# Performance work log

Measured on AMD Instinct MI355X. Metric: run time of the kernel, lower is better.

The kernel has to match this reference:

```python
import jax, jax.numpy as jnp
import numpy as np

N_NODES = 100000
N_EDGES = 1600000
DIM_IN, DIM_H, DIM_OUT = 64, 64, 16


def setup_inputs() -> dict:
    key = jax.random.key(0)
    ks = jax.random.split(key, 7)
    s = lambda d: 1.0 / np.sqrt(d)
    return {
        "x": jax.random.normal(ks[0], (N_NODES, DIM_IN), dtype=jnp.float32),
        "edge_index": jax.random.randint(ks[1], (2, N_EDGES), 0, N_NODES, dtype=jnp.int32),
        "W1l": jax.random.normal(ks[2], (DIM_IN, DIM_H), dtype=jnp.float32) * s(DIM_IN),
        "W1r": jax.random.normal(ks[3], (DIM_IN, DIM_H), dtype=jnp.float32) * s(DIM_IN),
        "b1": jnp.zeros((DIM_H,), dtype=jnp.float32),
        "W2l": jax.random.normal(ks[4], (DIM_H, DIM_OUT), dtype=jnp.float32) * s(DIM_H),
        "W2r": jax.random.normal(ks[5], (DIM_H, DIM_OUT), dtype=jnp.float32) * s(DIM_H),
        "b2": jnp.zeros((DIM_OUT,), dtype=jnp.float32),
    }


def _sage_conv(h, edge_index, Wl, Wr, b):
    # PyG SAGEConv (mean aggr): out = mean_{j in N(i)} h_j @ Wl + h_i @ Wr + b
    src, dst = edge_index[0], edge_index[1]
    n = h.shape[0]
    agg = jax.ops.segment_sum(h[src], dst, num_segments=n)          # [N, d]
    deg = jax.ops.segment_sum(jnp.ones_like(dst, dtype=h.dtype), dst, num_segments=n)
    mean = agg / jnp.maximum(deg, 1.0)[:, None]
    return mean @ Wl + h @ Wr + b


def reference(x, edge_index, W1l, W1r, b1, W2l, W2r, b2):
    h = jax.nn.relu(_sage_conv(x, edge_index, W1l, W1r, b1))
    # dropout(p=0.5) is identity in eval mode (training=False)
    h = _sage_conv(h, edge_index, W2l, W2r, b2)
    return jax.nn.log_softmax(h, axis=1)
```

## Files before the change

kernel.cpp:

```cpp
#include <hip/hip_runtime.h>
#include <cstdint>
#include <cstddef>


typedef float f32x4 __attribute__((ext_vector_type(4)));
typedef float f32x2 __attribute__((ext_vector_type(2)));
typedef short short8 __attribute__((ext_vector_type(8)));
typedef __bf16 bf16x8 __attribute__((ext_vector_type(8)));

#define BK 256
#define NBMAX 512
#define CAP 5120
#define TILE 8192

__device__ __forceinline__ unsigned f2bf(float f) {
    unsigned u = __float_as_uint(f);
    u += 0x7FFFu + ((u >> 16) & 1u);
    return u >> 16;
}

__device__ __forceinline__ f32x4 mfma16(short8 a, short8 b, f32x4 c) {
    return __builtin_amdgcn_mfma_f32_16x16x32_bf16(
        __builtin_bit_cast(bf16x8, a), __builtin_bit_cast(bf16x8, b), c, 0, 0, 0);
}

#define ACC2(r, alo, ahi)                     \
    alo += __uint_as_float((r) << 16);        \
    ahi += __uint_as_float(r);

#define ACCF8(w, i)                                                   \
    {                                                                 \
        f32x2 f0 = __builtin_amdgcn_cvt_pk_f32_fp8((w), false);       \
        f32x2 f1 = __builtin_amdgcn_cvt_pk_f32_fp8((w), true);        \
        acc[(i)] += f0.x; acc[(i) + 1] += f0.y;                       \
        acc[(i) + 2] += f1.x; acc[(i) + 3] += f1.y;                   \
    }

__global__ __launch_bounds__(512) void partprep_k(
    const int* __restrict__ ei, int* __restrict__ bcnt,
    unsigned* __restrict__ part, int E, int pblocks,
    const float* __restrict__ x, unsigned short* __restrict__ xb,
    unsigned char* __restrict__ xq, int n,
    const float* __restrict__ W1l, const float* __restrict__ W1r,
    const float* __restrict__ W2l, const float* __restrict__ W2r,
    unsigned short* __restrict__ bimg, int xblocks) {
    __shared__ int scn[NBMAX], sbase[NBMAX], lofs[NBMAX], cur[NBMAX];
    __shared__ unsigned stageW[TILE];
    __shared__ unsigned short stageB[TILE];
    int t = threadIdx.x;
    int bid = blockIdx.x;

    if (bid >= pblocks) {
        int cb = bid - pblocks;
        if (cb < xblocks) {
            int i = (cb * 512 + t) * 8;
            if (i >= n) return;
            const float4* xp = (const float4*)(x + i);
            float4 a = xp[0], b = xp[1];
            uint4 o;
            o.x = f2bf(a.x) | (f2bf(a.y) << 16);
            o.y = f2bf(a.z) | (f2bf(a.w) << 16);
            o.z = f2bf(b.x) | (f2bf(b.y) << 16);
            o.w = f2bf(b.z) | (f2bf(b.w) << 16);
            *(uint4*)(xb + i) = o;
            int w0 = __builtin_amdgcn_cvt_pk_fp8_f32(a.x, a.y, 0, false);
            w0 = __builtin_amdgcn_cvt_pk_fp8_f32(a.z, a.w, w0, true);
            int w1 = __builtin_amdgcn_cvt_pk_fp8_f32(b.x, b.y, 0, false);
            w1 = __builtin_amdgcn_cvt_pk_fp8_f32(b.z, b.w, w1, true);
            *(uint2*)(xq + i) = make_uint2((unsigned)w0, (unsigned)w1);
            return;
        }
        int e = (cb - xblocks) * 512 + t;
        if (e >= 20 * 64) return;
        int f = e >> 6, L = e & 63;
        int qd = L >> 4, m = L & 15;
        unsigned o[8];
        if (f < 16) {
            int kb = f >> 2, nb = f & 3;
            int n2 = nb * 16 + m;
#pragma unroll
            for (int j = 0; j < 8; ++j) {
                int k = kb * 32 + qd * 8 + j;
                float v = (k < 64) ? W1l[k * 64 + n2] : W1r[(k - 64) * 64 + n2];
                o[j] = f2bf(v);
            }
        } else {
            int g = f - 16;
            int kb = g >> 1, nb = g & 1;
#pragma unroll
            for (int j = 0; j < 8; ++j) {
                int k = kb * 32 + qd * 8 + j;
                float v = nb ? W2r[k * 16 + m] : W2l[k * 16 + m];
                o[j] = f2bf(v);
            }
        }
        uint4 pk;
        pk.x = o[0] | (o[1] << 16);
        pk.y = o[2] | (o[3] << 16);
        pk.z = o[4] | (o[5] << 16);
        pk.w = o[6] | (o[7] << 16);
        ((uint4*)bimg)[e] = pk;
        return;
    }

    int base = bid * TILE;
    cur[t] = 0;
    __syncthreads();
    int4 s4[4], d4[4];
#pragma unroll
    for (int i = 0; i < 4; ++i) {
        int e0 = base + (t + i * 512) * 4;
        if (e0 < E) {
            s4[i] = ((const int4*)ei)[e0 >> 2];
            d4[i] = ((const int4*)(ei + E))[e0 >> 2];
        } else {
            d4[i] = make_int4(-1, -1, -1, -1);
            s4[i] = make_int4(0, 0, 0, 0);
        }
    }
    int rk[16];
#pragma unroll
    for (int i = 0; i < 4; ++i) {
        int d[4] = {d4[i].x, d4[i].y, d4[i].z, d4[i].w};
#pragma unroll
        for (int u = 0; u < 4; ++u)
            rk[i * 4 + u] = (d[u] >= 0) ? atomicAdd(&cur[d[u] >> 8], 1) : 0;
    }
    __syncthreads();
    int own = cur[t];
    scn[t] = own;
    __syncthreads();
    for (int off = 1; off < NBMAX; off <<= 1) {
        int v = (t >= off) ? scn[t - off] : 0;
        __syncthreads();
        scn[t] += v;
        __syncthreads();
    }
    lofs[t] = scn[t] - own;
    if (own > 0) sbase[t] = atomicAdd(&bcnt[t], own);
    __syncthreads();
#pragma unroll
    for (int i = 0; i < 4; ++i) {
        int s[4] = {s4[i].x, s4[i].y, s4[i].z, s4[i].w};
        int d[4] = {d4[i].x, d4[i].y, d4[i].z, d4[i].w};
#pragma unroll
        for (int u = 0; u < 4; ++u) {
            if (d[u] < 0) continue;
            int b = d[u] >> 8;
            int pos = lofs[b] + rk[i * 4 + u];
            stageW[pos] = ((unsigned)(d[u] & (BK - 1)) << 17) | (unsigned)s[u];
            stageB[pos] = (unsigned short)b;
        }
    }
    __syncthreads();
    int tot = scn[NBMAX - 1];
    for (int q = t; q < tot; q += 512) {
        int b = stageB[q];
        part[b * CAP + sbase[b] + (q - lofs[b])] = stageW[q];
    }
}

__global__ __launch_bounds__(256) void csr_k(const unsigned* __restrict__ part,
                                             const int* __restrict__ bcnt,
                                             int* __restrict__ csr,
                                             int2* __restrict__ rowse, int N) {
    __shared__ int h[BK];
    __shared__ int s[BK];
    int b = blockIdx.x, t = threadIdx.x;
    int cnt = bcnt[b];
    int base = b * CAP;
    h[t] = 0;
    __syncthreads();
    for (int q = t; q < cnt; q += 256)
        atomicAdd(&h[(part[base + q] >> 17) & (BK - 1)], 1);
    __syncthreads();
    int own = h[t];
    s[t] = own;
    __syncthreads();
    for (int off = 1; off < BK; off <<= 1) {
        int v = (t >= off) ? s[t - off] : 0;
        __syncthreads();
        s[t] += v;
        __syncthreads();
    }
    int excl = s[t] - own;
    int node = b * BK + t;
    if (node < N) rowse[node] = make_int2(base + excl, base + excl + own);
    __syncthreads();
    h[t] = excl;
    __syncthreads();
    for (int q = t; q < cnt; q += 256) {
        unsigned w = part[base + q];
        int pos = atomicAdd(&h[(w >> 17) & (BK - 1)], 1);
        csr[base + pos] = (int)(w & 0x1FFFFu);
    }
}

__global__ __launch_bounds__(256, 6) void l1x(
    const unsigned short* __restrict__ xb, const unsigned char* __restrict__ xq,
    const int2* __restrict__ rowse, const int* __restrict__ csr,
    const unsigned short* __restrict__ bimg,
    const float* __restrict__ b1, const float* __restrict__ b2,
    unsigned short* __restrict__ p, float* __restrict__ q, int N) {
    __shared__ unsigned short mh[4][16][72];
    int t = threadIdx.x;
    int wave = t >> 6, lane = t & 63;
    int nodebase = blockIdx.x * 64 + wave * 16;
    int grp = lane >> 2, sub = lane & 3;
    int node = nodebase + grp;
    int2 be = (node < N) ? rowse[node] : make_int2(0, 0);

    float acc[16];
#pragma unroll
    for (int i = 0; i < 16; ++i) acc[i] = 0.f;
    int k = be.x, kend = be.y;
    for (; k + 1 < kend; k += 2) {
        int src0 = csr[k], src1 = csr[k + 1];
        uint4 a = ((const uint4*)(xq + ((size_t)src0 << 6)))[sub];
        uint4 b = ((const uint4*)(xq + ((size_t)src1 << 6)))[sub];
        ACCF8(a.x, 0); ACCF8(a.y, 4); ACCF8(a.z, 8); ACCF8(a.w, 12);
        ACCF8(b.x, 0); ACCF8(b.y, 4); ACCF8(b.z, 8); ACCF8(b.w, 12);
    }
    if (k < kend) {
        int src0 = csr[k];
        uint4 a = ((const uint4*)(xq + ((size_t)src0 << 6)))[sub];
        ACCF8(a.x, 0); ACCF8(a.y, 4); ACCF8(a.z, 8); ACCF8(a.w, 12);
    }
    {
        float rd = 1.0f / fmaxf((float)(be.y - be.x), 1.0f);
        uint4 o0, o1;
        o0.x = f2bf(acc[0] * rd) | (f2bf(acc[1] * rd) << 16);
        o0.y = f2bf(acc[2] * rd) | (f2bf(acc[3] * rd) << 16);
        o0.z = f2bf(acc[4] * rd) | (f2bf(acc[5] * rd) << 16);
        o0.w = f2bf(acc[6] * rd) | (f2bf(acc[7] * rd) << 16);
        o1.x = f2bf(acc[8] * rd) | (f2bf(acc[9] * rd) << 16);
        o1.y = f2bf(acc[10] * rd) | (f2bf(acc[11] * rd) << 16);
        o1.z = f2bf(acc[12] * rd) | (f2bf(acc[13] * rd) << 16);
        o1.w = f2bf(acc[14] * rd) | (f2bf(acc[15] * rd) << 16);
        *(uint4*)&mh[wave][grp][sub * 16] = o0;
        *(uint4*)&mh[wave][grp][sub * 16 + 8] = o1;
    }

    int qd = lane >> 4, m = lane & 15;
    int mynode = nodebase + m;
    const short8* bfr = (const short8*)bimg;
    short8 afr0 = *(const short8*)&mh[wave][m][qd * 8];
    short8 afr1 = *(const short8*)&mh[wave][m][32 + qd * 8];
    short8 afr2 = {0, 0, 0, 0, 0, 0, 0, 0};
    short8 afr3 = {0, 0, 0, 0, 0, 0, 0, 0};
    if (mynode < N) {
        afr2 = *(const short8*)(xb + ((size_t)mynode << 6) + qd * 8);
        afr3 = *(const short8*)(xb + ((size_t)mynode << 6) + 32 + qd * 8);
    }

#pragma unroll
    for (int nb = 0; nb < 4; ++nb) {
        f32x4 c = {0.f, 0.f, 0.f, 0.f};
        c = mfma16(afr0, bfr[nb * 64 + lane], c);
        c = mfma16(afr1, bfr[(4 + nb) * 64 + lane], c);
        c = mfma16(afr2, bfr[(8 + nb) * 64 + lane], c);
        c = mfma16(afr3, bfr[(12 + nb) * 64 + lane], c);
        int col = nb * 16 + m;
        float bb = b1[col];
#pragma unroll
        for (int r = 0; r < 4; ++r) {
            float hv = fmaxf(c[r] + bb, 0.0f);
            mh[wave][qd * 4 + r][col] = (unsigned short)f2bf(hv);
        }
    }

    short8 ha0 = *(const short8*)&mh[wave][m][qd * 8];
    short8 ha1 = *(const short8*)&mh[wave][m][32 + qd * 8];
    f32x4 pc = {0.f, 0.f, 0.f, 0.f}, qc = {0.f, 0.f, 0.f, 0.f};
    pc = mfma16(ha0, bfr[16 * 64 + lane], pc);
    pc = mfma16(ha1, bfr[18 * 64 + lane], pc);
    qc = mfma16(ha0, bfr[17 * 64 + lane], qc);
    qc = mfma16(ha1, bfr[19 * 64 + lane], qc);
    float b2v = b2[m];
#pragma unroll
    for (int r = 0; r < 4; ++r) {
        int nd = nodebase + qd * 4 + r;
        if (nd < N) {
            p[(size_t)nd * 16 + m] = (unsigned short)f2bf(pc[r]);
            q[(size_t)nd * 16 + m] = qc[r] + b2v;
        }
    }
}

__global__ __launch_bounds__(256) void finalk(const unsigned short* __restrict__ p,
                                              const int2* __restrict__ rowse,
                                              const int* __restrict__ csr,
                                              float* q, int N) {
    int t = threadIdx.x;
    int wave = t >> 6, lane = t & 63;
    int grp = lane >> 2, sub = lane & 3;
    int node = blockIdx.x * 64 + wave * 16 + grp;
    if (node >= N) return;
    int2 be = rowse[node];
    float a0 = 0.f, a1 = 0.f, a2 = 0.f, a3 = 0.f;
    int k = be.x, kend = be.y;
    for (; k + 1 < kend; k += 2) {
        int src0 = csr[k], src1 = csr[k + 1];
        uint2 rA = *(const uint2*)(p + ((size_t)src0 << 4) + (sub << 2));
        uint2 rB = *(const uint2*)(p + ((size_t)src1 << 4) + (sub << 2));
        ACC2(rA.x, a0, a1);  ACC2(rA.y, a2, a3);
        ACC2(rB.x, a0, a1);  ACC2(rB.y, a2, a3);
    }
    if (k < kend) {
        int src0 = csr[k];
        uint2 rA = *(const uint2*)(p + ((size_t)src0 << 4) + (sub << 2));
        ACC2(rA.x, a0, a1);  ACC2(rA.y, a2, a3);
    }
    float rd = 1.0f / fmaxf((float)(be.y - be.x), 1.0f);
    float4 qv = ((const float4*)(q + ((size_t)node << 4)))[sub];
    float4 v = {a0 * rd + qv.x, a1 * rd + qv.y, a2 * rd + qv.z, a3 * rd + qv.w};
    float mm = fmaxf(fmaxf(v.x, v.y), fmaxf(v.z, v.w));
    mm = fmaxf(mm, __shfl_xor(mm, 1));
    mm = fmaxf(mm, __shfl_xor(mm, 2));
    float s = __expf(v.x - mm) + __expf(v.y - mm) + __expf(v.z - mm) + __expf(v.w - mm);
    s += __shfl_xor(s, 1);
    s += __shfl_xor(s, 2);
    float ls = __logf(s);
    float4 o = {v.x - mm - ls, v.y - mm - ls, v.z - mm - ls, v.w - mm - ls};
    ((float4*)(q + ((size_t)node << 4)))[sub] = o;
}

extern "C" void kernel_launch(void* const* d_in, const int* in_sizes, int n_in,
                              void* d_out, int out_size, void* d_ws, size_t ws_size,
                              hipStream_t stream) {
    const float* x   = (const float*)d_in[0];
    const int* ei    = (const int*)d_in[1];
    const float* W1l = (const float*)d_in[2];
    const float* W1r = (const float*)d_in[3];
    const float* b1  = (const float*)d_in[4];
    const float* W2l = (const float*)d_in[5];
    const float* W2r = (const float*)d_in[6];
    const float* b2  = (const float*)d_in[7];
    const int N = in_sizes[0] / 64;
    const int E = in_sizes[1] / 2;
    const int nbk = (N + BK - 1) / BK;

    int*  bcnt  = (int*)d_ws;
    int2* rowse = (int2*)(bcnt + NBMAX);
    int*  csr   = (int*)(rowse + N);
    unsigned short* bimg = (unsigned short*)(csr + (size_t)nbk * CAP);
    unsigned short* p    = bimg + 20 * 64 * 8;
    unsigned* part = (unsigned*)(p + (size_t)N * 16);
    unsigned short* xb = (unsigned short*)(part + (size_t)nbk * CAP);
    unsigned char* xq = (unsigned char*)(xb + (size_t)N * 64);
    float* q = (float*)d_out;

    hipMemsetAsync(bcnt, 0, NBMAX * sizeof(int), stream);

    const int pblocks = (E + TILE - 1) / TILE;
    const int xblocks = (N * 64 + 4095) / 4096;
    partprep_k<<<pblocks + xblocks + 3, 512, 0, stream>>>(
        ei, bcnt, part, E, pblocks, x, xb, xq, N * 64, W1l, W1r, W2l, W2r,
        bimg, xblocks);
    csr_k<<<nbk, 256, 0, stream>>>(part, bcnt, csr, rowse, N);
    l1x<<<(N + 63) / 64, 256, 0, stream>>>(xb, xq, rowse, csr, bimg, b1, b2,
                                           p, q, N);
    finalk<<<(N + 63) / 64, 256, 0, stream>>>(p, rowse, csr, q, N);
}
```

Baseline: 161.0 us.

## Store layer-2 neighbor projections as fp8 and unroll gathers by four

The per-node layer-2 projection p is now written as fp8 bytes instead of bf16, which halves the bytes gathered per edge in the final aggregation kernel. Both gather loops (l1x and finalk) are unrolled from two to four neighbors per iteration so more loads are in flight at once. The cost is extra precision loss on the second-layer aggregation, which may hurt accuracy against the reference. The workspace offset for later buffers also shifts because p is smaller.

```diff
diff --git a/kernel.cpp b/kernel.cpp
--- a/kernel.cpp
+++ b/kernel.cpp
@@ -23,10 +23,6 @@
     return __builtin_amdgcn_mfma_f32_16x16x32_bf16(
         __builtin_bit_cast(bf16x8, a), __builtin_bit_cast(bf16x8, b), c, 0, 0, 0);
 }
-
-#define ACC2(r, alo, ahi)                     \
-    alo += __uint_as_float((r) << 16);        \
-    ahi += __uint_as_float(r);
 
 #define ACCF8(w, i)                                                   \
     {                                                                 \
@@ -34,6 +30,12 @@
         f32x2 f1 = __builtin_amdgcn_cvt_pk_f32_fp8((w), true);        \
         acc[(i)] += f0.x; acc[(i) + 1] += f0.y;                       \
         acc[(i) + 2] += f1.x; acc[(i) + 3] += f1.y;                   \
+    }
+#define ACCF8S(w)                                                     \
+    {                                                                 \
+        f32x2 f0 = __builtin_amdgcn_cvt_pk_f32_fp8((w), false);       \
+        f32x2 f1 = __builtin_amdgcn_cvt_pk_f32_fp8((w), true);        \
+        a0 += f0.x; a1 += f0.y; a2 += f1.x; a3 += f1.y;               \
     }
 
 __global__ __launch_bounds__(512) void partprep_k(
@@ -201,7 +203,7 @@
     const int2* __restrict__ rowse, const int* __restrict__ csr,
     const unsigned short* __restrict__ bimg,
     const float* __restrict__ b1, const float* __restrict__ b2,
-    unsigned short* __restrict__ p, float* __restrict__ q, int N) {
+    unsigned char* __restrict__ p, float* __restrict__ q, int N) {
     __shared__ unsigned short mh[4][16][72];
     int t = threadIdx.x;
     int wave = t >> 6, lane = t & 63;
@@ -214,14 +216,18 @@
 #pragma unroll
     for (int i = 0; i < 16; ++i) acc[i] = 0.f;
     int k = be.x, kend = be.y;
-    for (; k + 1 < kend; k += 2) {
-        int src0 = csr[k], src1 = csr[k + 1];
+    for (; k + 3 < kend; k += 4) {
+        int src0 = csr[k], src1 = csr[k + 1], src2 = csr[k + 2], src3 = csr[k + 3];
         uint4 a = ((const uint4*)(xq + ((size_t)src0 << 6)))[sub];
         uint4 b = ((const uint4*)(xq + ((size_t)src1 << 6)))[sub];
+        uint4 c = ((const uint4*)(xq + ((size_t)src2 << 6)))[sub];
+        uint4 d = ((const uint4*)(xq + ((size_t)src3 << 6)))[sub];
         ACCF8(a.x, 0); ACCF8(a.y, 4); ACCF8(a.z, 8); ACCF8(a.w, 12);
         ACCF8(b.x, 0); ACCF8(b.y, 4); ACCF8(b.z, 8); ACCF8(b.w, 12);
-    }
-    if (k < kend) {
+        ACCF8(c.x, 0); ACCF8(c.y, 4); ACCF8(c.z, 8); ACCF8(c.w, 12);
+        ACCF8(d.x, 0); ACCF8(d.y, 4); ACCF8(d.z, 8); ACCF8(d.w, 12);
+    }
+    for (; k < kend; ++k) {
         int src0 = csr[k];
         uint4 a = ((const uint4*)(xq + ((size_t)src0 << 6)))[sub];
         ACCF8(a.x, 0); ACCF8(a.y, 4); ACCF8(a.z, 8); ACCF8(a.w, 12);
@@ -281,13 +287,15 @@
     for (int r = 0; r < 4; ++r) {
         int nd = nodebase + qd * 4 + r;
         if (nd < N) {
-            p[(size_t)nd * 16 + m] = (unsigned short)f2bf(pc[r]);
+            unsigned pw = (unsigned)__builtin_amdgcn_cvt_pk_fp8_f32(
+                pc[r], pc[r], 0, false);
+            p[(size_t)nd * 16 + m] = (unsigned char)(pw & 0xFF);
             q[(size_t)nd * 16 + m] = qc[r] + b2v;
         }
     }
 }
 
-__global__ __launch_bounds__(256) void finalk(const unsigned short* __restrict__ p,
+__global__ __launch_bounds__(256) void finalk(const unsigned char* __restrict__ p,
                                               const int2* __restrict__ rowse,
                                               const int* __restrict__ csr,
                                               float* q, int N) {
@@ -299,17 +307,17 @@
     int2 be = rowse[node];
     float a0 = 0.f, a1 = 0.f, a2 = 0.f, a3 = 0.f;
     int k = be.x, kend = be.y;
-    for (; k + 1 < kend; k += 2) {
-        int src0 = csr[k], src1 = csr[k + 1];
-        uint2 rA = *(const uint2*)(p + ((size_t)src0 << 4) + (sub << 2));
-        uint2 rB = *(const uint2*)(p + ((size_t)src1 << 4) + (sub << 2));
-        ACC2(rA.x, a0, a1);  ACC2(rA.y, a2, a3);
-        ACC2(rB.x, a0, a1);  ACC2(rB.y, a2, a3);
-    }
-    if (k < kend) {
-        int src0 = csr[k];
-        uint2 rA = *(const uint2*)(p + ((size_t)src0 << 4) + (sub << 2));
-        ACC2(rA.x, a0, a1);  ACC2(rA.y, a2, a3);
+    for (; k + 3 < kend; k += 4) {
+        int src0 = csr[k], src1 = csr[k + 1], src2 = csr[k + 2], src3 = csr[k + 3];
+        unsigned rA = ((const unsigned*)(p + ((size_t)src0 << 4)))[sub];
+        unsigned rB = ((const unsigned*)(p + ((size_t)src1 << 4)))[sub];
+        unsigned rC = ((const unsigned*)(p + ((size_t)src2 << 4)))[sub];
+        unsigned rD = ((const unsigned*)(p + ((size_t)src3 << 4)))[sub];
+        ACCF8S(rA); ACCF8S(rB); ACCF8S(rC); ACCF8S(rD);
+    }
+    for (; k < kend; ++k) {
+        unsigned rA = ((const unsigned*)(p + ((size_t)csr[k] << 4)))[sub];
+        ACCF8S(rA);
     }
     float rd = 1.0f / fmaxf((float)(be.y - be.x), 1.0f);
     float4 qv = ((const float4*)(q + ((size_t)node << 4)))[sub];
@@ -344,7 +352,7 @@
     int2* rowse = (int2*)(bcnt + NBMAX);
     int*  csr   = (int*)(rowse + N);
     unsigned short* bimg = (unsigned short*)(csr + (size_t)nbk * CAP);
-    unsigned short* p    = bimg + 20 * 64 * 8;
+    unsigned char* p = (unsigned char*)(bimg + 20 * 64 * 8);
     unsigned* part = (unsigned*)(p + (size_t)N * 16);
     unsigned short* xb = (unsigned short*)(part + (size_t)nbk * CAP);
     unsigned char* xq = (unsigned char*)(xb + (size_t)N * 64);
```

Result: slower. 179.8 us (+11.7%).
